# Kernel optimization log

Hardware: AMD Instinct MI355X
Metric: run time of the kernel (lower is better)

## Reference

```python
import jax, jax.numpy as jnp
import numpy as np

MESSAGE_PASSES = 3  # constants.message_passes
F_NODE = 64   # hidden_node_features
F_EDGE = 16   # n_edge_features
M_MSG = 64    # message_size
OUT_DIM = 128
B, N = 8, 256
EDGE_DENSITY = 0.1


def setup_inputs() -> dict:
    key = jax.random.key(0)
    ks = jax.random.split(key, 12)
    nodes = jax.random.normal(ks[0], (B, N, F_NODE), dtype=jnp.float32)
    # sparse positive edge features: rand * bernoulli connectivity (avg degree ~ N*density)
    raw = jax.random.uniform(ks[1], (B, N, N, F_EDGE), dtype=jnp.float32)
    conn = (jax.random.uniform(ks[2], (B, N, N)) < EDGE_DENSITY).astype(jnp.float32)
    edges = raw * conn[..., None]
    s = 0.05
    return {
        "nodes": nodes,
        "edges": edges,
        # message MLP: cat(neighbour, edge) -> message_size
        "W_msg": jax.random.normal(ks[3], (F_NODE + F_EDGE, M_MSG), dtype=jnp.float32) * s,
        "b_msg": jnp.zeros((M_MSG,), dtype=jnp.float32),
        # GRU cell (input=message_size, hidden=F_NODE), gates [r|z|n]
        "W_i": jax.random.normal(ks[4], (M_MSG, 3 * F_NODE), dtype=jnp.float32) * s,
        "W_h": jax.random.normal(ks[5], (F_NODE, 3 * F_NODE), dtype=jnp.float32) * s,
        "b_i": jnp.zeros((3 * F_NODE,), dtype=jnp.float32),
        "b_h": jnp.zeros((3 * F_NODE,), dtype=jnp.float32),
        # gated readout
        "W_g": jax.random.normal(ks[6], (2 * F_NODE, OUT_DIM), dtype=jnp.float32) * s,
        "b_g": jnp.zeros((OUT_DIM,), dtype=jnp.float32),
        "W_e": jax.random.normal(ks[7], (F_NODE, OUT_DIM), dtype=jnp.float32) * s,
        "b_e": jnp.zeros((OUT_DIM,), dtype=jnp.float32),
    }


def reference(nodes, edges, W_msg, b_msg, W_i, W_h, b_i, b_h, W_g, b_g, W_e, b_e):
    # adjacency[b,i,j] != 0  <=>  edge (i<-j) exists (original: edges.sum(3).nonzero)
    adjacency = edges.sum(axis=-1)                                   # (B,N,N)
    nbr_mask = (adjacency != 0).astype(nodes.dtype)                  # (B,N,N)
    node_mask = (adjacency.sum(axis=-1) != 0)                        # (B,N) bool
    node_mask_f = node_mask.astype(nodes.dtype)

    h = nodes                                                        # hidden_nodes init = nodes
    b, n, f = nodes.shape
    for _ in range(MESSAGE_PASSES):
        # message_terms over all (node i, neighbour j) pairs; masked sum == padded-gather sum
        nghb = jnp.broadcast_to(h[:, None, :, :], (b, n, n, f))      # (B,N,N,F) neighbour feats
        feat = jnp.concatenate([nghb, edges], axis=-1)               # (B,N,N,F+E)
        terms = jax.nn.relu(feat @ W_msg + b_msg)                    # (B,N,N,M)
        messages = jnp.einsum('bijm,bij->bim', terms, nbr_mask)      # summation aggregation
        # GRU cell update
        gi = messages @ W_i + b_i                                    # (B,N,3F)
        gh = h @ W_h + b_h
        ir, iz, inn = jnp.split(gi, 3, axis=-1)
        hr, hz, hn = jnp.split(gh, 3, axis=-1)
        r = jax.nn.sigmoid(ir + hr)
        z = jax.nn.sigmoid(iz + hz)
        ng = jnp.tanh(inn + r * hn)
        h_new = (1.0 - z) * ng + z * h
        # only nodes with nonzero degree are scattered back (original indexes node_batch idc)
        h = jnp.where(node_mask[..., None], h_new, h)

    # gated readout: sum_i mask_i * sigmoid(g([h_i, x_i])) * e(h_i)
    gate = jax.nn.sigmoid(jnp.concatenate([h, nodes], axis=-1) @ W_g + b_g)  # (B,N,OUT)
    emb = h @ W_e + b_e                                                      # (B,N,OUT)
    out = jnp.einsum('bno,bn->bo', gate * emb, node_mask_f)                  # (B,OUT)
    return out
```

## Files before the change

### kernel.cpp

```cpp
#include <hip/hip_runtime.h>
#include <hip/hip_bf16.h>

#define BB 8
#define NN 256
#define FF 64
#define EE 16
#define MM 64
#define G3 192
#define OUTD 128
#define ROWS (BB*NN)
#define MAXD 64
#define RPB 4

__device__ __forceinline__ float sigmoidf_(float x) {
    return 1.0f / (1.0f + __expf(-x));
}

__global__ __launch_bounds__(256) void k_prep(
    const float* __restrict__ nodes, const float* __restrict__ edges,
    const float* __restrict__ Wmsg, const float* __restrict__ bmsg,
    int* __restrict__ deg, int* __restrict__ nbr,
    float* __restrict__ h, float* __restrict__ hn,
    float* __restrict__ edot, float* __restrict__ out)
{
    int row = blockIdx.x;
    int tid = threadIdx.x;
    int lane = tid & 63, wv = tid >> 6;
    __shared__ int wcnt[4];
    __shared__ int sdg;
    __shared__ float snode[FF];
    __shared__ float efeat[MAXD][EE];

    const float4* ep = (const float4*)(edges + (((size_t)row) * NN + tid) * EE);
    float4 a = ep[0], b4 = ep[1], c4 = ep[2], d4 = ep[3];
    float s = a.x+a.y+a.z+a.w + b4.x+b4.y+b4.z+b4.w
            + c4.x+c4.y+c4.z+c4.w + d4.x+d4.y+d4.z+d4.w;
    bool pred = (s != 0.0f);
    unsigned long long m = __ballot(pred);
    if (lane == 0) wcnt[wv] = __popcll(m);
    if (tid < FF) snode[tid] = nodes[(size_t)row * FF + tid];
    __syncthreads();

    int base = 0;
    #pragma unroll
    for (int q = 0; q < 4; ++q) base += (q < wv) ? wcnt[q] : 0;
    int slot = base + __popcll(m & ((1ull << lane) - 1ull));
    if (pred && slot < MAXD) {
        nbr[row * MAXD + slot] = tid;
        float4* dst = (float4*)&efeat[slot][0];
        dst[0] = a; dst[1] = b4; dst[2] = c4; dst[3] = d4;
    }
    if (tid == 0) {
        int tot = wcnt[0] + wcnt[1] + wcnt[2] + wcnt[3];
        sdg = (tot < MAXD) ? tot : MAXD;
        deg[row] = sdg;
    }
    __syncthreads();

    if (tid < FF) h[row * FF + tid] = snode[tid];
    if (tid < MM) {
        float acc = bmsg[tid];
        #pragma unroll 8
        for (int k = 0; k < FF; ++k) acc += snode[k] * Wmsg[k * MM + tid];
        hn[row * MM + tid] = acc;
    }

    float we[EE];
    #pragma unroll
    for (int k = 0; k < EE; ++k) we[k] = Wmsg[(FF + k) * MM + lane];

    int d = sdg;
    float* ed = edot + (size_t)row * MAXD * MM;
    for (int sl = wv; sl < d; sl += 4) {
        float acc = 0.0f;
        #pragma unroll
        for (int k = 0; k < EE; ++k) acc += efeat[sl][k] * we[k];
        ed[sl * MM + lane] = acc;
    }

    if (row == 0) {
        #pragma unroll
        for (int i = 0; i < (BB * OUTD) / 256; ++i) out[i * 256 + tid] = 0.0f;
    }
}

__global__ __launch_bounds__(1024, 8) void k_pass4(
    const float* __restrict__ Wmsg, const float* __restrict__ bmsg,
    const float* __restrict__ Wi, const float* __restrict__ Wh,
    const float* __restrict__ bi, const float* __restrict__ bh,
    const float* __restrict__ nodes,
    const float* __restrict__ Wg, const float* __restrict__ bg,
    const float* __restrict__ We, const float* __restrict__ be,
    const int* __restrict__ deg, const int* __restrict__ nbr,
    const float* __restrict__ edot,
    const float* __restrict__ hn_in, float* __restrict__ hn_out,
    float* __restrict__ h, float* __restrict__ out, int last)
{
    const int r0   = blockIdx.x * RPB;
    const int b    = r0 >> 8;
    const int tid  = threadIdx.x;
    const int w    = tid >> 6;
    const int lane = tid & 63;

    __shared__ int   snbr[RPB][MAXD];
    __shared__ int   sdeg[RPB];
    __shared__ float part[16][MM];
    __shared__ float smsg[RPB][MM];
    __shared__ float sh[RPB][FF];
    __shared__ float sx[RPB][FF];
    __shared__ float pg[6][2][RPB][FF];
    __shared__ float sg[RPB][OUTD];
    __shared__ float se[RPB][OUTD];

    if (tid < RPB) sdeg[tid] = deg[r0 + tid];
    if (tid < RPB * MAXD) {
        snbr[tid >> 6][tid & 63] = nbr[(r0 + (tid >> 6)) * MAXD + (tid & 63)];
    } else if (tid < 2 * RPB * MAXD) {
        int x = tid - RPB * MAXD;
        sh[x >> 6][x & 63] = h[(size_t)(r0 + (x >> 6)) * FF + (x & 63)];
    } else if (last && tid < 3 * RPB * MAXD) {
        int x = tid - 2 * RPB * MAXD;
        sx[x >> 6][x & 63] = nodes[(size_t)(r0 + (x >> 6)) * FF + (x & 63)];
    }
    __syncthreads();

    {
        int r = w >> 2, sub = w & 3;
        int d = sdeg[r];
        const float* hb = hn_in + (size_t)b * NN * MM;
        const float* ed = edot + (size_t)(r0 + r) * MAXD * MM;
        float acc = 0.0f;
        for (int s = sub; s < d; s += 4) {
            int j = snbr[r][s];
            acc += fmaxf(hb[j * MM + lane] + ed[s * MM + lane], 0.0f);
        }
        part[w][lane] = acc;
    }
    __syncthreads();
    if (tid < RPB * MM) {
        int r = tid >> 6, tt = tid & 63;
        smsg[r][tt] = part[r*4][tt] + part[r*4+1][tt] + part[r*4+2][tt] + part[r*4+3][tt];
    }
    __syncthreads();

    if (w < 12) {
        int g = w >> 1, kh = w & 1;
        float a0 = 0, a1 = 0, a2 = 0, a3 = 0;
        if (g < 3) {
            for (int k = kh * 32; k < kh * 32 + 32; ++k) {
                float wgt = Wi[k * G3 + g * FF + lane];
                a0 += smsg[0][k] * wgt; a1 += smsg[1][k] * wgt;
                a2 += smsg[2][k] * wgt; a3 += smsg[3][k] * wgt;
            }
        } else {
            int gg = g - 3;
            for (int k = kh * 32; k < kh * 32 + 32; ++k) {
                float wgt = Wh[k * G3 + gg * FF + lane];
                a0 += sh[0][k] * wgt; a1 += sh[1][k] * wgt;
                a2 += sh[2][k] * wgt; a3 += sh[3][k] * wgt;
            }
        }
        pg[g][kh][0][lane] = a0; pg[g][kh][1][lane] = a1;
        pg[g][kh][2][lane] = a2; pg[g][kh][3][lane] = a3;
    }
    __syncthreads();

    if (tid < RPB * FF) {
        int r = tid >> 6, tt = tid & 63;
        float ir  = bi[tt]          + pg[0][0][r][tt] + pg[0][1][r][tt];
        float iz  = bi[FF + tt]     + pg[1][0][r][tt] + pg[1][1][r][tt];
        float in_ = bi[2*FF + tt]   + pg[2][0][r][tt] + pg[2][1][r][tt];
        float hr  = bh[tt]          + pg[3][0][r][tt] + pg[3][1][r][tt];
        float hz  = bh[FF + tt]     + pg[4][0][r][tt] + pg[4][1][r][tt];
        float hnn = bh[2*FF + tt]   + pg[5][0][r][tt] + pg[5][1][r][tt];
        float rr = sigmoidf_(ir + hr);
        float zz = sigmoidf_(iz + hz);
        float ng = tanhf(in_ + rr * hnn);
        float hold = sh[r][tt];
        float hnew = (1.0f - zz) * ng + zz * hold;
        if (sdeg[r] == 0) hnew = hold;
        sh[r][tt] = hnew;
        if (!last) h[(size_t)(r0 + r) * FF + tt] = hnew;
    }
    __syncthreads();

    if (!last) {
        if (w < 4) {
            float a0 = 0, a1 = 0, a2 = 0, a3 = 0;
            #pragma unroll
            for (int kk = 0; kk < 16; ++kk) {
                int k = w * 16 + kk;
                float wgt = Wmsg[k * MM + lane];
                a0 += sh[0][k] * wgt; a1 += sh[1][k] * wgt;
                a2 += sh[2][k] * wgt; a3 += sh[3][k] * wgt;
            }
            part[w*4+0][lane] = a0; part[w*4+1][lane] = a1;
            part[w*4+2][lane] = a2; part[w*4+3][lane] = a3;
        }
        __syncthreads();
        if (tid < RPB * MM) {
            int r = tid >> 6, tt = tid & 63;
            hn_out[(size_t)(r0 + r) * MM + tt] = bmsg[tt]
                + part[0*4+r][tt] + part[1*4+r][tt] + part[2*4+r][tt] + part[3*4+r][tt];
        }
    } else {
        int grp = tid >> 7, o = tid & 127;
        int r = grp >> 1, kind = grp & 1;
        if (kind == 0) {
            float g = bg[o];
            #pragma unroll 4
            for (int k = 0; k < FF; ++k) g += sh[r][k] * Wg[k * OUTD + o];
            #pragma unroll 4
            for (int k = 0; k < FF; ++k) g += sx[r][k] * Wg[(FF + k) * OUTD + o];
            sg[r][o] = g;
        } else {
            float e = be[o];
            #pragma unroll 4
            for (int k = 0; k < FF; ++k) e += sh[r][k] * We[k * OUTD + o];
            se[r][o] = e;
        }
        __syncthreads();
        if (tid < OUTD) {
            float v = 0.0f;
            #pragma unroll
            for (int r2 = 0; r2 < RPB; ++r2)
                v += (sdeg[r2] != 0) ? sigmoidf_(sg[r2][tid]) * se[r2][tid] : 0.0f;
            atomicAdd(&out[b * OUTD + tid], v);
        }
    }
}

extern "C" void kernel_launch(void* const* d_in, const int* in_sizes, int n_in,
                              void* d_out, int out_size, void* d_ws, size_t ws_size,
                              hipStream_t stream) {
    const float* nodes = (const float*)d_in[0];
    const float* edges = (const float*)d_in[1];
    const float* Wmsg  = (const float*)d_in[2];
    const float* bmsg  = (const float*)d_in[3];
    const float* Wi    = (const float*)d_in[4];
    const float* Wh    = (const float*)d_in[5];
    const float* bi    = (const float*)d_in[6];
    const float* bh    = (const float*)d_in[7];
    const float* Wg    = (const float*)d_in[8];
    const float* bg    = (const float*)d_in[9];
    const float* We    = (const float*)d_in[10];
    const float* be    = (const float*)d_in[11];
    float* out = (float*)d_out;
    char* ws = (char*)d_ws;

    int*   deg  = (int*)ws;
    int*   nbr  = (int*)(ws + 8192);
    float* h    = (float*)(ws + 8192 + (size_t)ROWS * MAXD * 4);
    float* hnA  = h    + (size_t)ROWS * FF;
    float* hnB  = hnA  + (size_t)ROWS * MM;
    float* edot = hnB  + (size_t)ROWS * MM;

    k_prep<<<ROWS, 256, 0, stream>>>(nodes, edges, Wmsg, bmsg, deg, nbr,
                                     h, hnA, edot, out);

    k_pass4<<<ROWS/RPB, 1024, 0, stream>>>(Wmsg, bmsg, Wi, Wh, bi, bh,
                                           nodes, Wg, bg, We, be, deg, nbr, edot,
                                           hnA, hnB, h, out, 0);
    k_pass4<<<ROWS/RPB, 1024, 0, stream>>>(Wmsg, bmsg, Wi, Wh, bi, bh,
                                           nodes, Wg, bg, We, be, deg, nbr, edot,
                                           hnB, hnA, h, out, 0);
    k_pass4<<<ROWS/RPB, 1024, 0, stream>>>(Wmsg, bmsg, Wi, Wh, bi, bh,
                                           nodes, Wg, bg, We, be, deg, nbr, edot,
                                           hnA, hnB, h, out, 1);
}
```

Measured before the change: 152.1 us.

## Recompute edge projections per pass instead of materialising edot buffer

Drops the precomputed per-edge projection buffer (edot, ROWS*64*64 floats) that k_prep wrote and each pass re-read. Each pass now gathers the sparse neighbours' raw 16-float edge features into shared memory and recomputes the 16-term dot product inline. The pass kernel also shrinks to 512 threads, with the GRU gate and readout work reassigned across fewer waves. This cuts global write and read traffic in exchange for redundant edge math in three passes and fewer threads per block.

```diff
diff --git a/kernel.cpp b/kernel.cpp
--- a/kernel.cpp
+++ b/kernel.cpp
@@ -20,16 +20,13 @@
     const float* __restrict__ nodes, const float* __restrict__ edges,
     const float* __restrict__ Wmsg, const float* __restrict__ bmsg,
     int* __restrict__ deg, int* __restrict__ nbr,
-    float* __restrict__ h, float* __restrict__ hn,
-    float* __restrict__ edot, float* __restrict__ out)
+    float* __restrict__ h, float* __restrict__ hn, float* __restrict__ out)
 {
     int row = blockIdx.x;
     int tid = threadIdx.x;
     int lane = tid & 63, wv = tid >> 6;
     __shared__ int wcnt[4];
-    __shared__ int sdg;
     __shared__ float snode[FF];
-    __shared__ float efeat[MAXD][EE];
 
     const float4* ep = (const float4*)(edges + (((size_t)row) * NN + tid) * EE);
     float4 a = ep[0], b4 = ep[1], c4 = ep[2], d4 = ep[3];
@@ -45,18 +42,12 @@
     #pragma unroll
     for (int q = 0; q < 4; ++q) base += (q < wv) ? wcnt[q] : 0;
     int slot = base + __popcll(m & ((1ull << lane) - 1ull));
-    if (pred && slot < MAXD) {
-        nbr[row * MAXD + slot] = tid;
-        float4* dst = (float4*)&efeat[slot][0];
-        dst[0] = a; dst[1] = b4; dst[2] = c4; dst[3] = d4;
-    }
+    if (pred && slot < MAXD) nbr[row * MAXD + slot] = tid;
+
     if (tid == 0) {
         int tot = wcnt[0] + wcnt[1] + wcnt[2] + wcnt[3];
-        sdg = (tot < MAXD) ? tot : MAXD;
-        deg[row] = sdg;
-    }
-    __syncthreads();
-
+        deg[row] = (tot < MAXD) ? tot : MAXD;
+    }
     if (tid < FF) h[row * FF + tid] = snode[tid];
     if (tid < MM) {
         float acc = bmsg[tid];
@@ -64,27 +55,14 @@
         for (int k = 0; k < FF; ++k) acc += snode[k] * Wmsg[k * MM + tid];
         hn[row * MM + tid] = acc;
     }
-
-    float we[EE];
-    #pragma unroll
-    for (int k = 0; k < EE; ++k) we[k] = Wmsg[(FF + k) * MM + lane];
-
-    int d = sdg;
-    float* ed = edot + (size_t)row * MAXD * MM;
-    for (int sl = wv; sl < d; sl += 4) {
-        float acc = 0.0f;
-        #pragma unroll
-        for (int k = 0; k < EE; ++k) acc += efeat[sl][k] * we[k];
-        ed[sl * MM + lane] = acc;
-    }
-
     if (row == 0) {
         #pragma unroll
         for (int i = 0; i < (BB * OUTD) / 256; ++i) out[i * 256 + tid] = 0.0f;
     }
 }
 
-__global__ __launch_bounds__(1024, 8) void k_pass4(
+__global__ __launch_bounds__(512, 8) void k_pass4(
+    const float* __restrict__ edges,
     const float* __restrict__ Wmsg, const float* __restrict__ bmsg,
     const float* __restrict__ Wi, const float* __restrict__ Wh,
     const float* __restrict__ bi, const float* __restrict__ bh,
@@ -92,7 +70,6 @@
     const float* __restrict__ Wg, const float* __restrict__ bg,
     const float* __restrict__ We, const float* __restrict__ be,
     const int* __restrict__ deg, const int* __restrict__ nbr,
-    const float* __restrict__ edot,
     const float* __restrict__ hn_in, float* __restrict__ hn_out,
     float* __restrict__ h, float* __restrict__ out, int last)
 {
@@ -104,78 +81,94 @@
 
     __shared__ int   snbr[RPB][MAXD];
     __shared__ int   sdeg[RPB];
-    __shared__ float part[16][MM];
+    __shared__ float efeat[RPB][MAXD][EE];
+    __shared__ float part[8][MM];
     __shared__ float smsg[RPB][MM];
     __shared__ float sh[RPB][FF];
     __shared__ float sx[RPB][FF];
-    __shared__ float pg[6][2][RPB][FF];
+    __shared__ float pg[6][RPB][FF];
     __shared__ float sg[RPB][OUTD];
     __shared__ float se[RPB][OUTD];
 
     if (tid < RPB) sdeg[tid] = deg[r0 + tid];
     if (tid < RPB * MAXD) {
         snbr[tid >> 6][tid & 63] = nbr[(r0 + (tid >> 6)) * MAXD + (tid & 63)];
-    } else if (tid < 2 * RPB * MAXD) {
+        if (last) {
+            int r = tid >> 6, k = tid & 63;
+            sx[r][k] = nodes[(size_t)(r0 + r) * FF + k];
+        }
+    } else {
         int x = tid - RPB * MAXD;
         sh[x >> 6][x & 63] = h[(size_t)(r0 + (x >> 6)) * FF + (x & 63)];
-    } else if (last && tid < 3 * RPB * MAXD) {
-        int x = tid - 2 * RPB * MAXD;
-        sx[x >> 6][x & 63] = nodes[(size_t)(r0 + (x >> 6)) * FF + (x & 63)];
+    }
+
+    float we[EE];
+    #pragma unroll
+    for (int k = 0; k < EE; ++k) we[k] = Wmsg[(FF + k) * MM + lane];
+    __syncthreads();
+
+    #pragma unroll
+    for (int r = 0; r < RPB; ++r) {
+        int cnt4 = sdeg[r] * 4;
+        for (int i = tid; i < cnt4; i += 512) {
+            int slot = i >> 2, q = i & 3;
+            const float4* src =
+                (const float4*)(edges + (((size_t)(r0 + r)) * NN + snbr[r][slot]) * EE);
+            ((float4*)&efeat[r][slot][0])[q] = src[q];
+        }
     }
     __syncthreads();
 
     {
-        int r = w >> 2, sub = w & 3;
+        int r = w >> 1, sub = w & 1;
         int d = sdeg[r];
         const float* hb = hn_in + (size_t)b * NN * MM;
-        const float* ed = edot + (size_t)(r0 + r) * MAXD * MM;
         float acc = 0.0f;
-        for (int s = sub; s < d; s += 4) {
+        for (int s = sub; s < d; s += 2) {
             int j = snbr[r][s];
-            acc += fmaxf(hb[j * MM + lane] + ed[s * MM + lane], 0.0f);
+            float term = hb[j * MM + lane];
+            #pragma unroll
+            for (int k = 0; k < EE; ++k) term += efeat[r][s][k] * we[k];
+            acc += fmaxf(term, 0.0f);
         }
         part[w][lane] = acc;
     }
     __syncthreads();
     if (tid < RPB * MM) {
         int r = tid >> 6, tt = tid & 63;
-        smsg[r][tt] = part[r*4][tt] + part[r*4+1][tt] + part[r*4+2][tt] + part[r*4+3][tt];
-    }
-    __syncthreads();
-
-    if (w < 12) {
-        int g = w >> 1, kh = w & 1;
-        float a0 = 0, a1 = 0, a2 = 0, a3 = 0;
-        if (g < 3) {
-            for (int k = kh * 32; k < kh * 32 + 32; ++k) {
-                float wgt = Wi[k * G3 + g * FF + lane];
-                a0 += smsg[0][k] * wgt; a1 += smsg[1][k] * wgt;
-                a2 += smsg[2][k] * wgt; a3 += smsg[3][k] * wgt;
-            }
-        } else {
-            int gg = g - 3;
-            for (int k = kh * 32; k < kh * 32 + 32; ++k) {
-                float wgt = Wh[k * G3 + gg * FF + lane];
-                a0 += sh[0][k] * wgt; a1 += sh[1][k] * wgt;
-                a2 += sh[2][k] * wgt; a3 += sh[3][k] * wgt;
-            }
-        }
-        pg[g][kh][0][lane] = a0; pg[g][kh][1][lane] = a1;
-        pg[g][kh][2][lane] = a2; pg[g][kh][3][lane] = a3;
+        smsg[r][tt] = part[2*r][tt] + part[2*r+1][tt];
+    }
+    __syncthreads();
+
+    if (w < 3) {
+        float a0 = bi[w * FF + lane], a1 = a0, a2 = a0, a3 = a0;
+        #pragma unroll 4
+        for (int k = 0; k < FF; ++k) {
+            float wgt = Wi[k * G3 + w * FF + lane];
+            a0 += smsg[0][k] * wgt; a1 += smsg[1][k] * wgt;
+            a2 += smsg[2][k] * wgt; a3 += smsg[3][k] * wgt;
+        }
+        pg[w][0][lane] = a0; pg[w][1][lane] = a1;
+        pg[w][2][lane] = a2; pg[w][3][lane] = a3;
+    } else if (w < 6) {
+        int g = w - 3;
+        float a0 = bh[g * FF + lane], a1 = a0, a2 = a0, a3 = a0;
+        #pragma unroll 4
+        for (int k = 0; k < FF; ++k) {
+            float wgt = Wh[k * G3 + g * FF + lane];
+            a0 += sh[0][k] * wgt; a1 += sh[1][k] * wgt;
+            a2 += sh[2][k] * wgt; a3 += sh[3][k] * wgt;
+        }
+        pg[3 + g][0][lane] = a0; pg[3 + g][1][lane] = a1;
+        pg[3 + g][2][lane] = a2; pg[3 + g][3][lane] = a3;
     }
     __syncthreads();
 
     if (tid < RPB * FF) {
         int r = tid >> 6, tt = tid & 63;
-        float ir  = bi[tt]          + pg[0][0][r][tt] + pg[0][1][r][tt];
-        float iz  = bi[FF + tt]     + pg[1][0][r][tt] + pg[1][1][r][tt];
-        float in_ = bi[2*FF + tt]   + pg[2][0][r][tt] + pg[2][1][r][tt];
-        float hr  = bh[tt]          + pg[3][0][r][tt] + pg[3][1][r][tt];
-        float hz  = bh[FF + tt]     + pg[4][0][r][tt] + pg[4][1][r][tt];
-        float hnn = bh[2*FF + tt]   + pg[5][0][r][tt] + pg[5][1][r][tt];
-        float rr = sigmoidf_(ir + hr);
-        float zz = sigmoidf_(iz + hz);
-        float ng = tanhf(in_ + rr * hnn);
+        float rr = sigmoidf_(pg[0][r][tt] + pg[3][r][tt]);
+        float zz = sigmoidf_(pg[1][r][tt] + pg[4][r][tt]);
+        float ng = tanhf(pg[2][r][tt] + rr * pg[5][r][tt]);
         float hold = sh[r][tt];
         float hnew = (1.0f - zz) * ng + zz * hold;
         if (sdeg[r] == 0) hnew = hold;
@@ -185,40 +178,34 @@
     __syncthreads();
 
     if (!last) {
-        if (w < 4) {
-            float a0 = 0, a1 = 0, a2 = 0, a3 = 0;
+        {
+            int r = w >> 1, kh = w & 1;
+            float p = 0.0f;
             #pragma unroll
-            for (int kk = 0; kk < 16; ++kk) {
-                int k = w * 16 + kk;
-                float wgt = Wmsg[k * MM + lane];
-                a0 += sh[0][k] * wgt; a1 += sh[1][k] * wgt;
-                a2 += sh[2][k] * wgt; a3 += sh[3][k] * wgt;
+            for (int kk = 0; kk < 32; ++kk) {
+                int k = kh * 32 + kk;
+                p += sh[r][k] * Wmsg[k * MM + lane];
             }
-            part[w*4+0][lane] = a0; part[w*4+1][lane] = a1;
-            part[w*4+2][lane] = a2; part[w*4+3][lane] = a3;
+            part[w][lane] = p;
         }
         __syncthreads();
         if (tid < RPB * MM) {
             int r = tid >> 6, tt = tid & 63;
             hn_out[(size_t)(r0 + r) * MM + tt] = bmsg[tt]
-                + part[0*4+r][tt] + part[1*4+r][tt] + part[2*4+r][tt] + part[3*4+r][tt];
+                + part[2*r][tt] + part[2*r+1][tt];
         }
     } else {
-        int grp = tid >> 7, o = tid & 127;
-        int r = grp >> 1, kind = grp & 1;
-        if (kind == 0) {
-            float g = bg[o];
-            #pragma unroll 4
-            for (int k = 0; k < FF; ++k) g += sh[r][k] * Wg[k * OUTD + o];
-            #pragma unroll 4
-            for (int k = 0; k < FF; ++k) g += sx[r][k] * Wg[(FF + k) * OUTD + o];
-            sg[r][o] = g;
-        } else {
-            float e = be[o];
-            #pragma unroll 4
-            for (int k = 0; k < FF; ++k) e += sh[r][k] * We[k * OUTD + o];
-            se[r][o] = e;
-        }
+        int r = tid >> 7, o = tid & 127;
+        float g = bg[o], e = be[o];
+        #pragma unroll 4
+        for (int k = 0; k < FF; ++k) {
+            float hk = sh[r][k];
+            g += hk * Wg[k * OUTD + o];
+            e += hk * We[k * OUTD + o];
+        }
+        #pragma unroll 4
+        for (int k = 0; k < FF; ++k) g += sx[r][k] * Wg[(FF + k) * OUTD + o];
+        sg[r][o] = g; se[r][o] = e;
         __syncthreads();
         if (tid < OUTD) {
             float v = 0.0f;
@@ -251,20 +238,18 @@
     int*   deg  = (int*)ws;
     int*   nbr  = (int*)(ws + 8192);
     float* h    = (float*)(ws + 8192 + (size_t)ROWS * MAXD * 4);
-    float* hnA  = h    + (size_t)ROWS * FF;
-    float* hnB  = hnA  + (size_t)ROWS * MM;
-    float* edot = hnB  + (size_t)ROWS * MM;
-
-    k_prep<<<ROWS, 256, 0, stream>>>(nodes, edges, Wmsg, bmsg, deg, nbr,
-                                     h, hnA, edot, out);
-
-    k_pass4<<<ROWS/RPB, 1024, 0, stream>>>(Wmsg, bmsg, Wi, Wh, bi, bh,
-                                           nodes, Wg, bg, We, be, deg, nbr, edot,
-                                           hnA, hnB, h, out, 0);
-    k_pass4<<<ROWS/RPB, 1024, 0, stream>>>(Wmsg, bmsg, Wi, Wh, bi, bh,
-                                           nodes, Wg, bg, We, be, deg, nbr, edot,
-                                           hnB, hnA, h, out, 0);
-    k_pass4<<<ROWS/RPB, 1024, 0, stream>>>(Wmsg, bmsg, Wi, Wh, bi, bh,
-                                           nodes, Wg, bg, We, be, deg, nbr, edot,
-                                           hnA, hnB, h, out, 1);
-}
+    float* hnA  = h   + (size_t)ROWS * FF;
+    float* hnB  = hnA + (size_t)ROWS * MM;
+
+    k_prep<<<ROWS, 256, 0, stream>>>(nodes, edges, Wmsg, bmsg, deg, nbr, h, hnA, out);
+
+    k_pass4<<<ROWS/RPB, 512, 0, stream>>>(edges, Wmsg, bmsg, Wi, Wh, bi, bh,
+                                          nodes, Wg, bg, We, be, deg, nbr,
+                                          hnA, hnB, h, out, 0);
+    k_pass4<<<ROWS/RPB, 512, 0, stream>>>(edges, Wmsg, bmsg, Wi, Wh, bi, bh,
+                                          nodes, Wg, bg, We, be, deg, nbr,
+                                          hnB, hnA, h, out, 0);
+    k_pass4<<<ROWS/RPB, 512, 0, stream>>>(edges, Wmsg, bmsg, Wi, Wh, bi, bh,
+                                          nodes, Wg, bg, We, be, deg, nbr,
+                                          hnA, hnB, h, out, 1);
+}
```

Result: no change. 151.3 us (-0.5%).
